# Optimization experiments

Measured on AMD Instinct MI355X. Metric: run time of the kernel, lower is better.

Reference implementation:

```python
import jax, jax.numpy as jnp
import numpy as np

NEG_SLOPE = 0.2


def gat_conv(x, src, dst, n, W, a_src, a_dst, b):
    # x: [N, Din], W: [Din, Dout], a_src/a_dst: [Dout], b: [Dout]
    h = x @ W                                   # [N, Dout]
    alpha_src = h @ a_src                       # [N] score contribution of source nodes
    alpha_dst = h @ a_dst                       # [N]
    e = jax.nn.leaky_relu(alpha_src[src] + alpha_dst[dst], NEG_SLOPE)  # [E]
    # segment softmax over destination nodes (every node has a self-loop -> no empty segs)
    m = jax.ops.segment_max(e, dst, num_segments=n)
    p = jnp.exp(e - m[dst])
    denom = jax.ops.segment_sum(p, dst, num_segments=n)
    coeff = p / denom[dst]                      # [E]
    out = jax.ops.segment_sum(h[src] * coeff[:, None], dst, num_segments=n)
    return out + b


def setup_inputs() -> dict:
    key = jax.random.key(0)
    ks = jax.random.split(key, 16)
    N, E, D_IN, D_H, C = 50000, 800000, 256, 256, 10
    x = jax.random.normal(ks[0], (N, D_IN), dtype=jnp.float32)
    edge_index = jax.random.randint(ks[1], (2, E), 0, N, dtype=jnp.int64)
    s = 0.1
    params = {
        "W1": jax.random.normal(ks[2], (D_IN, D_H), jnp.float32) * s,
        "a_src1": jax.random.normal(ks[3], (D_H,), jnp.float32) * s,
        "a_dst1": jax.random.normal(ks[4], (D_H,), jnp.float32) * s,
        "b1": jnp.zeros((D_H,), jnp.float32),
        "W2": jax.random.normal(ks[5], (D_H, D_H), jnp.float32) * s,
        "a_src2": jax.random.normal(ks[6], (D_H,), jnp.float32) * s,
        "a_dst2": jax.random.normal(ks[7], (D_H,), jnp.float32) * s,
        "b2": jnp.zeros((D_H,), jnp.float32),
        "W3": jax.random.normal(ks[8], (D_H, C), jnp.float32) * s,
        "a_src3": jax.random.normal(ks[9], (C,), jnp.float32) * s,
        "a_dst3": jax.random.normal(ks[10], (C,), jnp.float32) * s,
        "b3": jnp.zeros((C,), jnp.float32),
    }
    return {"x": x, "edge_index": edge_index, **params}


def reference(x, edge_index, W1, a_src1, a_dst1, b1, W2, a_src2, a_dst2, b2,
              W3, a_src3, a_dst3, b3):
    n = x.shape[0]
    # PyG GATConv default add_self_loops=True
    loops = jnp.arange(n, dtype=edge_index.dtype)
    src = jnp.concatenate([edge_index[0], loops])
    dst = jnp.concatenate([edge_index[1], loops])
    h = gat_conv(x, src, dst, n, W1, a_src1, a_dst1, b1)
    h = jax.nn.relu(h)
    h = gat_conv(h, src, dst, n, W2, a_src2, a_dst2, b2)
    h = jax.nn.relu(h)
    out = gat_conv(h, src, dst, n, W3, a_src3, a_dst3, b3)
    return out
```

## Files before the change

kernel.cpp:

```cpp
#include <hip/hip_runtime.h>
#include <math.h>

#define N_NODES 50000
#define N_EDGES 800000
#define EP (N_EDGES + N_NODES)
#define NEG_SLOPE 0.2f
#define SCAN_BLOCKS ((N_NODES + 255) / 256)

typedef short short8 __attribute__((ext_vector_type(8)));
typedef float float4_ __attribute__((ext_vector_type(4)));

__device__ __forceinline__ unsigned short f2bf(float f) {
  unsigned int u = __float_as_uint(f);
  u = (u + 0x7FFFu + ((u >> 16) & 1u)) >> 16;
  return (unsigned short)u;
}
__device__ __forceinline__ float bf2f(unsigned int us) {
  return __uint_as_float(us << 16);
}
__device__ __forceinline__ unsigned int pack2(float lo, float hi) {
  return (unsigned int)f2bf(lo) | ((unsigned int)f2bf(hi) << 16);
}

__device__ __forceinline__ int permc(int p) {
  return ((p & 0xE) << 4) | ((p & 1) << 4) | (p >> 4);
}


template <int PERM>
__global__ void cvt_wf_kernel(const float* __restrict__ W, unsigned short* __restrict__ Wf) {
  int t = blockIdx.x * 256 + threadIdx.x;
  int f = t >> 6, lane = t & 63;
  int nt = f >> 3, k0t = f & 7;
  int lm = lane & 15, kg = lane >> 4;
  int kbase = k0t * 32 + kg * 8;
  int n = nt * 16 + lm;
  short8 v;
#pragma unroll
  for (int j = 0; j < 8; ++j) {
    int k = PERM ? permc(kbase + j) : (kbase + j);
    v[j] = (short)f2bf(W[(size_t)k * 256 + n]);
  }
  ((short8*)Wf)[t] = v;
}

__global__ void cvt_wf3_kernel(const float* __restrict__ W3, unsigned short* __restrict__ Wf3) {
  int t = blockIdx.x * 256 + threadIdx.x;
  int k0t = t >> 6, lane = t & 63;
  int lm = lane & 15, kg = lane >> 4;
  int kbase = k0t * 32 + kg * 8;
  short8 v;
#pragma unroll
  for (int j = 0; j < 8; ++j) {
    int k = permc(kbase + j);
    v[j] = (lm < 10) ? (short)f2bf(W3[(size_t)k * 10 + lm]) : (short)0;
  }
  ((short8*)Wf3)[t] = v;
}

__global__ void permute_bias_kernel(const float* __restrict__ b1, const float* __restrict__ b2,
                                    float* __restrict__ pb1, float* __restrict__ pb2) {
  int p = threadIdx.x;
  int c = permc(p);
  pb1[p] = b1[c];
  pb2[p] = b2[c];
}


__global__ void count_kernel(const int* __restrict__ ei, int* __restrict__ cnt) {
  int e = blockIdx.x * 256 + threadIdx.x;
  if (e >= EP) return;
  int dst = (e < N_EDGES) ? ei[N_EDGES + e] : (e - N_EDGES);
  atomicAdd(&cnt[dst], 1);
}

__global__ void scan1_kernel(const int* __restrict__ cnt, int* __restrict__ off,
                             int* __restrict__ bsum) {
  int i = blockIdx.x * 256 + threadIdx.x;
  int v = (i < N_NODES) ? cnt[i] : 0;
  int lane = threadIdx.x & 63, w = threadIdx.x >> 6;
  int x = v;
  for (int o = 1; o < 64; o <<= 1) { int y = __shfl_up(x, o); if (lane >= o) x += y; }
  __shared__ int wsum[4];
  if (lane == 63) wsum[w] = x;
  __syncthreads();
  int add = 0;
  for (int k = 0; k < w; ++k) add += wsum[k];
  if (i < N_NODES) off[i] = x - v + add;
  if (threadIdx.x == 255) bsum[blockIdx.x] = add + x;
}

__global__ void scan2_kernel(int* __restrict__ bsum, int* __restrict__ bpre,
                             int* __restrict__ off) {
  int t = threadIdx.x;
  int v = (t < SCAN_BLOCKS) ? bsum[t] : 0;
  int lane = t & 63, w = t >> 6;
  int x = v;
  for (int o = 1; o < 64; o <<= 1) { int y = __shfl_up(x, o); if (lane >= o) x += y; }
  __shared__ int wsum[4];
  if (lane == 63) wsum[w] = x;
  __syncthreads();
  int add = 0;
  for (int k = 0; k < w; ++k) add += wsum[k];
  if (t < SCAN_BLOCKS) bpre[t] = x - v + add;
  if (t == 255) off[N_NODES] = add + x;
}

__global__ void scan3_kernel(int* __restrict__ off, const int* __restrict__ bpre) {
  int i = blockIdx.x * 256 + threadIdx.x;
  if (i < N_NODES) off[i] += bpre[blockIdx.x];
}

__global__ void scatter_kernel(const int* __restrict__ ei, const int* __restrict__ off,
                               int* __restrict__ cnt, int* __restrict__ esrc) {
  int e = blockIdx.x * 256 + threadIdx.x;
  if (e >= EP) return;
  int src, dst;
  if (e < N_EDGES) { src = ei[e]; dst = ei[N_EDGES + e]; }
  else { src = dst = e - N_EDGES; }
  int pos = off[dst] + atomicAdd(&cnt[dst], 1);
  esrc[pos] = src;
}


template <int AF32>
__global__ __launch_bounds__(512, 2) void gemm_mfma4(const void* __restrict__ Av,
                                                     const uint4* __restrict__ Wf,
                                                     unsigned short* __restrict__ C,
                                                     const float* __restrict__ asrc,
                                                     const float* __restrict__ adst,
                                                     float* __restrict__ as_,
                                                     float* __restrict__ ad_, int M) {
  __shared__ uint4 Bl[8192];
  int tid = threadIdx.x;
#pragma unroll
  for (int i = 0; i < 16; ++i) Bl[i * 512 + tid] = Wf[i * 512 + tid];
  int wave = tid >> 6, lane = tid & 63;
  int lm = lane & 15, kg = lane >> 4;
  int row0 = blockIdx.x * 256 + wave * 32;
  int ar0 = row0 + lm, ar1 = row0 + 16 + lm;
  if (ar0 >= M) ar0 = M - 1;
  if (ar1 >= M) ar1 = M - 1;
  float4_ acc0[16], acc1[16];
#pragma unroll
  for (int i = 0; i < 16; ++i) { acc0[i] = (float4_){0, 0, 0, 0}; acc1[i] = (float4_){0, 0, 0, 0}; }
  __syncthreads();
  const short8* Bf = (const short8*)Bl;
  for (int k0t = 0; k0t < 8; ++k0t) {
    int k0 = k0t * 32;
    short8 a0, a1;
    if (AF32) {
      const float* A = (const float*)Av;
      const float* p0 = A + (size_t)ar0 * 256 + kg * 8 + k0;
      const float* p1 = A + (size_t)ar1 * 256 + kg * 8 + k0;
      float4 f0 = *(const float4*)p0, f1 = *(const float4*)(p0 + 4);
      float4 g0 = *(const float4*)p1, g1 = *(const float4*)(p1 + 4);
      a0 = (short8){(short)f2bf(f0.x), (short)f2bf(f0.y), (short)f2bf(f0.z), (short)f2bf(f0.w),
                    (short)f2bf(f1.x), (short)f2bf(f1.y), (short)f2bf(f1.z), (short)f2bf(f1.w)};
      a1 = (short8){(short)f2bf(g0.x), (short)f2bf(g0.y), (short)f2bf(g0.z), (short)f2bf(g0.w),
                    (short)f2bf(g1.x), (short)f2bf(g1.y), (short)f2bf(g1.z), (short)f2bf(g1.w)};
    } else {
      const unsigned short* A = (const unsigned short*)Av;
      a0 = *(const short8*)(A + (size_t)ar0 * 256 + kg * 8 + k0);
      a1 = *(const short8*)(A + (size_t)ar1 * 256 + kg * 8 + k0);
    }
#pragma unroll
    for (int nt = 0; nt < 16; ++nt) {
      short8 b = Bf[(nt * 8 + k0t) * 64 + lane];
      acc0[nt] = __builtin_amdgcn_mfma_f32_16x16x32_bf16(a0, b, acc0[nt], 0, 0, 0);
      acc1[nt] = __builtin_amdgcn_mfma_f32_16x16x32_bf16(a1, b, acc1[nt], 0, 0, 0);
    }
  }
  float avs[16], avd[16];
#pragma unroll
  for (int nt = 0; nt < 16; ++nt) { avs[nt] = asrc[nt * 16 + lm]; avd[nt] = adst[nt * 16 + lm]; }
#pragma unroll
  for (int g = 0; g < 2; ++g) {
    int rbase = row0 + g * 16 + kg * 4;
#pragma unroll
    for (int i = 0; i < 4; ++i) {
      int r = rbase + i;
      float s = 0.f, dd = 0.f;
      unsigned int u[8];
#pragma unroll
      for (int j = 0; j < 8; ++j) {
        float vlo = g ? acc1[2 * j][i] : acc0[2 * j][i];
        float vhi = g ? acc1[2 * j + 1][i] : acc0[2 * j + 1][i];
        u[j] = pack2(vlo, vhi);
        s += vlo * avs[2 * j] + vhi * avs[2 * j + 1];
        dd += vlo * avd[2 * j] + vhi * avd[2 * j + 1];
      }
      if (r < M) {
        uint4* cp = (uint4*)(C + (size_t)r * 256 + lm * 16);
        cp[0] = (uint4){u[0], u[1], u[2], u[3]};
        cp[1] = (uint4){u[4], u[5], u[6], u[7]};
      }
#pragma unroll
      for (int o = 1; o < 16; o <<= 1) { s += __shfl_xor(s, o); dd += __shfl_xor(dd, o); }
      if (lm == 0 && r < M) { as_[r] = s; ad_[r] = dd; }
    }
  }
}


__global__ __launch_bounds__(256) void gemm_c3_kernel(const unsigned short* __restrict__ X,
                                                      const unsigned short* __restrict__ Wf3,
                                                      const float* __restrict__ asrc,
                                                      const float* __restrict__ adst,
                                                      float* __restrict__ h3,
                                                      float* __restrict__ as_,
                                                      float* __restrict__ ad_, int M) {
  int tid = threadIdx.x;
  int wave = tid >> 6, lane = tid & 63;
  int lm = lane & 15, kg = lane >> 4;
  int row0 = blockIdx.x * 128 + wave * 32;
  int ar0 = row0 + lm, ar1 = row0 + 16 + lm;
  if (ar0 >= M) ar0 = M - 1;
  if (ar1 >= M) ar1 = M - 1;
  short8 bf[8];
#pragma unroll
  for (int k0t = 0; k0t < 8; ++k0t) bf[k0t] = ((const short8*)Wf3)[k0t * 64 + lane];
  float4_ acc0 = (float4_){0, 0, 0, 0}, acc1 = (float4_){0, 0, 0, 0};
#pragma unroll
  for (int k0t = 0; k0t < 8; ++k0t) {
    int k0 = k0t * 32;
    short8 a0 = *(const short8*)(X + (size_t)ar0 * 256 + kg * 8 + k0);
    short8 a1 = *(const short8*)(X + (size_t)ar1 * 256 + kg * 8 + k0);
    acc0 = __builtin_amdgcn_mfma_f32_16x16x32_bf16(a0, bf[k0t], acc0, 0, 0, 0);
    acc1 = __builtin_amdgcn_mfma_f32_16x16x32_bf16(a1, bf[k0t], acc1, 0, 0, 0);
  }
  float avs = (lm < 10) ? asrc[lm] : 0.f;
  float avd = (lm < 10) ? adst[lm] : 0.f;
#pragma unroll
  for (int g = 0; g < 2; ++g) {
    int rbase = row0 + g * 16 + kg * 4;
#pragma unroll
    for (int i = 0; i < 4; ++i) {
      int r = rbase + i;
      float v = g ? acc1[i] : acc0[i];
      if (r < M && lm < 10) h3[(size_t)r * 10 + lm] = v;
      float s = v * avs, dd = v * avd;
#pragma unroll
      for (int o = 1; o < 16; o <<= 1) { s += __shfl_xor(s, o); dd += __shfl_xor(dd, o); }
      if (lm == 0 && r < M) { as_[r] = s; ad_[r] = dd; }
    }
  }
}


__global__ __launch_bounds__(256) void agg_fused_kernel(const int* __restrict__ off,
                                                        const int* __restrict__ esrc,
                                                        const float* __restrict__ as_,
                                                        const float* __restrict__ ad_,
                                                        const unsigned short* __restrict__ h,
                                                        const float* __restrict__ pbias,
                                                        unsigned short* __restrict__ outg) {
  __shared__ int s_src[4][64];
  __shared__ float s_p[4][64];
  int wave = threadIdx.x >> 6, lane = threadIdx.x & 63;
  int pair = lane >> 5, cl = lane & 31;
  int d = blockIdx.x * 4 + wave;
  int s0 = off[d], s1 = off[d + 1];
  float adv = ad_[d];
  const uint4* hp4 = (const uint4*)h;
  float a0 = 0.f, a1 = 0.f, a2 = 0.f, a3 = 0.f, a4 = 0.f, a5 = 0.f, a6 = 0.f, a7 = 0.f;
  float sum = 0.f;
  for (int base = s0; base < s1; base += 64) {
    int m = s1 - base; if (m > 64) m = 64;
    int sv = 0; float p = 0.f;
    if (lane < m) {
      sv = esrc[base + lane];
      float e = as_[sv] + adv;
      e = e > 0.f ? e : NEG_SLOPE * e;
      p = __expf(e);
    }
    s_src[wave][lane] = sv;
    s_p[wave][lane] = p;
    float ps = p;
    for (int o = 32; o; o >>= 1) ps += __shfl_xor(ps, o);
    sum += ps;
    int nb = (m + 1) >> 1;
    int j = 0;
    for (; j + 4 <= nb; j += 4) {
#pragma unroll
      for (int u = 0; u < 4; ++u) {
        int idx = (j + u) * 2 + pair;
        int src = s_src[wave][idx];
        float w = s_p[wave][idx];
        uint4 pv = hp4[(size_t)src * 32 + cl];
        a0 = fmaf(w, bf2f(pv.x & 0xffffu), a0); a1 = fmaf(w, bf2f(pv.x >> 16), a1);
        a2 = fmaf(w, bf2f(pv.y & 0xffffu), a2); a3 = fmaf(w, bf2f(pv.y >> 16), a3);
        a4 = fmaf(w, bf2f(pv.z & 0xffffu), a4); a5 = fmaf(w, bf2f(pv.z >> 16), a5);
        a6 = fmaf(w, bf2f(pv.w & 0xffffu), a6); a7 = fmaf(w, bf2f(pv.w >> 16), a7);
      }
    }
    for (; j < nb; ++j) {
      int idx = j * 2 + pair;
      int src = s_src[wave][idx];
      float w = s_p[wave][idx];
      uint4 pv = hp4[(size_t)src * 32 + cl];
      a0 = fmaf(w, bf2f(pv.x & 0xffffu), a0); a1 = fmaf(w, bf2f(pv.x >> 16), a1);
      a2 = fmaf(w, bf2f(pv.y & 0xffffu), a2); a3 = fmaf(w, bf2f(pv.y >> 16), a3);
      a4 = fmaf(w, bf2f(pv.z & 0xffffu), a4); a5 = fmaf(w, bf2f(pv.z >> 16), a5);
      a6 = fmaf(w, bf2f(pv.w & 0xffffu), a6); a7 = fmaf(w, bf2f(pv.w >> 16), a7);
    }
  }
  a0 += __shfl_xor(a0, 32); a1 += __shfl_xor(a1, 32);
  a2 += __shfl_xor(a2, 32); a3 += __shfl_xor(a3, 32);
  a4 += __shfl_xor(a4, 32); a5 += __shfl_xor(a5, 32);
  a6 += __shfl_xor(a6, 32); a7 += __shfl_xor(a7, 32);
  if (pair == 0) {
    float inv = 1.0f / sum;
    float4 b0 = ((const float4*)pbias)[2 * cl];
    float4 b1 = ((const float4*)pbias)[2 * cl + 1];
    float o0 = fmaxf(fmaf(a0, inv, b0.x), 0.f);
    float o1 = fmaxf(fmaf(a1, inv, b0.y), 0.f);
    float o2 = fmaxf(fmaf(a2, inv, b0.z), 0.f);
    float o3 = fmaxf(fmaf(a3, inv, b0.w), 0.f);
    float o4 = fmaxf(fmaf(a4, inv, b1.x), 0.f);
    float o5 = fmaxf(fmaf(a5, inv, b1.y), 0.f);
    float o6 = fmaxf(fmaf(a6, inv, b1.z), 0.f);
    float o7 = fmaxf(fmaf(a7, inv, b1.w), 0.f);
    uint4 ov = (uint4){pack2(o0, o1), pack2(o2, o3), pack2(o4, o5), pack2(o6, o7)};
    ((uint4*)outg)[(size_t)d * 32 + cl] = ov;
  }
}


__global__ void agg10_fused_kernel(const int* __restrict__ off, const int* __restrict__ esrc,
                                   const float* __restrict__ as_, const float* __restrict__ ad_,
                                   const float* __restrict__ h, const float* __restrict__ bias,
                                   float* __restrict__ out) {
  int gid = blockIdx.x * 256 + threadIdx.x;
  int wid = gid >> 6, lane = threadIdx.x & 63;
  int g = lane >> 4, c = lane & 15;
  int d = wid * 4 + g;
  if (d >= N_NODES) return;
  int s0 = off[d], s1 = off[d + 1];
  float adv = ad_[d];
  float acc = 0.f, sum = 0.f;
  int s = s0;
  for (; s + 2 <= s1; s += 2) {
    int i0 = esrc[s], i1 = esrc[s + 1];
    float e0 = as_[i0] + adv; e0 = e0 > 0.f ? e0 : NEG_SLOPE * e0;
    float e1 = as_[i1] + adv; e1 = e1 > 0.f ? e1 : NEG_SLOPE * e1;
    float h0 = (c < 10) ? h[(size_t)i0 * 10 + c] : 0.f;
    float h1 = (c < 10) ? h[(size_t)i1 * 10 + c] : 0.f;
    float p0 = __expf(e0), p1 = __expf(e1);
    acc = fmaf(p0, h0, acc);
    acc = fmaf(p1, h1, acc);
    sum += p0 + p1;
  }
  if (s < s1) {
    int i0 = esrc[s];
    float e0 = as_[i0] + adv; e0 = e0 > 0.f ? e0 : NEG_SLOPE * e0;
    float p0 = __expf(e0);
    if (c < 10) acc = fmaf(p0, h[(size_t)i0 * 10 + c], acc);
    sum += p0;
  }
  if (c < 10) out[(size_t)d * 10 + c] = fmaf(acc, 1.0f / sum, bias[c]);
}


extern "C" void kernel_launch(void* const* d_in, const int* in_sizes, int n_in,
                              void* d_out, int out_size, void* d_ws, size_t ws_size,
                              hipStream_t stream) {
  const float* x   = (const float*)d_in[0];
  const int*   ei  = (const int*)d_in[1];
  const float* W1  = (const float*)d_in[2];
  const float* as1 = (const float*)d_in[3];
  const float* ad1 = (const float*)d_in[4];
  const float* b1  = (const float*)d_in[5];
  const float* W2  = (const float*)d_in[6];
  const float* as2 = (const float*)d_in[7];
  const float* ad2 = (const float*)d_in[8];
  const float* b2  = (const float*)d_in[9];
  const float* W3  = (const float*)d_in[10];
  const float* as3 = (const float*)d_in[11];
  const float* ad3 = (const float*)d_in[12];
  const float* b3  = (const float*)d_in[13];
  float* out = (float*)d_out;

  char* ws = (char*)d_ws;
  size_t off_b = 0;
  auto alloc = [&](size_t bytes) -> char* {
    char* p = ws + off_b;
    off_b += (bytes + 255) & ~(size_t)255;
    return p;
  };
  unsigned short* hb   = (unsigned short*)alloc((size_t)N_NODES * 256 * 2);
  unsigned short* gb   = (unsigned short*)alloc((size_t)N_NODES * 256 * 2);
  unsigned short* Wf1  = (unsigned short*)alloc(256 * 256 * 2);
  unsigned short* Wf2  = (unsigned short*)alloc(256 * 256 * 2);
  unsigned short* Wf3  = (unsigned short*)alloc(8 * 64 * 8 * 2);
  float* pb1   = (float*)alloc(256 * 4);
  float* pb2   = (float*)alloc(256 * 4);
  float* h3    = (float*)alloc((size_t)N_NODES * 10 * 4);
  float* as_   = (float*)alloc((size_t)N_NODES * 4);
  float* ad_   = (float*)alloc((size_t)N_NODES * 4);
  int*   roff  = (int*)alloc((size_t)(N_NODES + 1) * 4);
  int*   cnt   = (int*)alloc((size_t)N_NODES * 4);
  int*   bsum  = (int*)alloc((size_t)SCAN_BLOCKS * 4);
  int*   bpre  = (int*)alloc((size_t)SCAN_BLOCKS * 4);
  int*   esrc  = (int*)alloc((size_t)EP * 4);

  cvt_wf_kernel<0><<<32, 256, 0, stream>>>(W1, Wf1);
  cvt_wf_kernel<1><<<32, 256, 0, stream>>>(W2, Wf2);
  cvt_wf3_kernel<<<2, 256, 0, stream>>>(W3, Wf3);
  permute_bias_kernel<<<1, 256, 0, stream>>>(b1, b2, pb1, pb2);

  hipMemsetAsync(cnt, 0, N_NODES * 4, stream);
  int eb = (EP + 255) / 256;
  count_kernel<<<eb, 256, 0, stream>>>(ei, cnt);
  scan1_kernel<<<SCAN_BLOCKS, 256, 0, stream>>>(cnt, roff, bsum);
  scan2_kernel<<<1, 256, 0, stream>>>(bsum, bpre, roff);
  scan3_kernel<<<SCAN_BLOCKS, 256, 0, stream>>>(roff, bpre);
  hipMemsetAsync(cnt, 0, N_NODES * 4, stream);
  scatter_kernel<<<eb, 256, 0, stream>>>(ei, roff, cnt, esrc);

  int g4blocks = (N_NODES + 255) / 256;
  int g3blocks = (N_NODES + 127) / 128;
  int ablocks = (N_NODES + 3) / 4;
  int wgrid4 = (N_NODES * 16 + 255) / 256;

  gemm_mfma4<1><<<g4blocks, 512, 0, stream>>>(x, (const uint4*)Wf1, hb, as1, ad1, as_, ad_, N_NODES);
  agg_fused_kernel<<<ablocks, 256, 0, stream>>>(roff, esrc, as_, ad_, hb, pb1, gb);
  gemm_mfma4<0><<<g4blocks, 512, 0, stream>>>(gb, (const uint4*)Wf2, hb, as2, ad2, as_, ad_, N_NODES);
  agg_fused_kernel<<<ablocks, 256, 0, stream>>>(roff, esrc, as_, ad_, hb, pb2, gb);
  gemm_c3_kernel<<<g3blocks, 256, 0, stream>>>(gb, Wf3, as3, ad3, h3, as_, ad_, N_NODES);
  agg10_fused_kernel<<<wgrid4, 256, 0, stream>>>(roff, esrc, as_, ad_, h3, b3, out);
}
```

Baseline: 379.3 us.

## Prefetch GEMM A tiles, pad layer-3 features, rewrite final aggregation per-wave

The MFMA GEMM now loads the next K-slice of A while the current slice's MFMAs run, hiding global load latency. Layer-3 features are stored padded to 16 floats per row so the final aggregation can fetch them as float4. That aggregation is rewritten to one wave per destination node, with edge weights staged in shared memory, 16 edges processed in parallel and a shuffle reduction. The unroll of the hidden-layer aggregation inner loop also goes from 4 to 8. Costs are more registers in the GEMM and extra memory traffic from the padded layout.

```diff
diff --git a/kernel.cpp b/kernel.cpp
--- a/kernel.cpp
+++ b/kernel.cpp
@@ -141,35 +141,36 @@
   int ar0 = row0 + lm, ar1 = row0 + 16 + lm;
   if (ar0 >= M) ar0 = M - 1;
   if (ar1 >= M) ar1 = M - 1;
+
+  auto loadA = [&](int k0t, int ar) -> short8 {
+    if (AF32) {
+      const float* A = (const float*)Av;
+      const float* p = A + (size_t)ar * 256 + kg * 8 + k0t * 32;
+      float4 f0 = *(const float4*)p, f1 = *(const float4*)(p + 4);
+      return (short8){(short)f2bf(f0.x), (short)f2bf(f0.y), (short)f2bf(f0.z), (short)f2bf(f0.w),
+                      (short)f2bf(f1.x), (short)f2bf(f1.y), (short)f2bf(f1.z), (short)f2bf(f1.w)};
+    } else {
+      const unsigned short* A = (const unsigned short*)Av;
+      return *(const short8*)(A + (size_t)ar * 256 + kg * 8 + k0t * 32);
+    }
+  };
+
   float4_ acc0[16], acc1[16];
 #pragma unroll
   for (int i = 0; i < 16; ++i) { acc0[i] = (float4_){0, 0, 0, 0}; acc1[i] = (float4_){0, 0, 0, 0}; }
+  short8 a0 = loadA(0, ar0), a1 = loadA(0, ar1);
   __syncthreads();
   const short8* Bf = (const short8*)Bl;
   for (int k0t = 0; k0t < 8; ++k0t) {
-    int k0 = k0t * 32;
-    short8 a0, a1;
-    if (AF32) {
-      const float* A = (const float*)Av;
-      const float* p0 = A + (size_t)ar0 * 256 + kg * 8 + k0;
-      const float* p1 = A + (size_t)ar1 * 256 + kg * 8 + k0;
-      float4 f0 = *(const float4*)p0, f1 = *(const float4*)(p0 + 4);
-      float4 g0 = *(const float4*)p1, g1 = *(const float4*)(p1 + 4);
-      a0 = (short8){(short)f2bf(f0.x), (short)f2bf(f0.y), (short)f2bf(f0.z), (short)f2bf(f0.w),
-                    (short)f2bf(f1.x), (short)f2bf(f1.y), (short)f2bf(f1.z), (short)f2bf(f1.w)};
-      a1 = (short8){(short)f2bf(g0.x), (short)f2bf(g0.y), (short)f2bf(g0.z), (short)f2bf(g0.w),
-                    (short)f2bf(g1.x), (short)f2bf(g1.y), (short)f2bf(g1.z), (short)f2bf(g1.w)};
-    } else {
-      const unsigned short* A = (const unsigned short*)Av;
-      a0 = *(const short8*)(A + (size_t)ar0 * 256 + kg * 8 + k0);
-      a1 = *(const short8*)(A + (size_t)ar1 * 256 + kg * 8 + k0);
-    }
+    short8 na0, na1;
+    if (k0t < 7) { na0 = loadA(k0t + 1, ar0); na1 = loadA(k0t + 1, ar1); }
 #pragma unroll
     for (int nt = 0; nt < 16; ++nt) {
       short8 b = Bf[(nt * 8 + k0t) * 64 + lane];
       acc0[nt] = __builtin_amdgcn_mfma_f32_16x16x32_bf16(a0, b, acc0[nt], 0, 0, 0);
       acc1[nt] = __builtin_amdgcn_mfma_f32_16x16x32_bf16(a1, b, acc1[nt], 0, 0, 0);
     }
+    a0 = na0; a1 = na1;
   }
   float avs[16], avd[16];
 #pragma unroll
@@ -207,7 +208,7 @@
                                                       const unsigned short* __restrict__ Wf3,
                                                       const float* __restrict__ asrc,
                                                       const float* __restrict__ adst,
-                                                      float* __restrict__ h3,
+                                                      float* __restrict__ h3p,
                                                       float* __restrict__ as_,
                                                       float* __restrict__ ad_, int M) {
   int tid = threadIdx.x;
@@ -238,7 +239,7 @@
     for (int i = 0; i < 4; ++i) {
       int r = rbase + i;
       float v = g ? acc1[i] : acc0[i];
-      if (r < M && lm < 10) h3[(size_t)r * 10 + lm] = v;
+      if (r < M) h3p[(size_t)r * 16 + lm] = v;
       float s = v * avs, dd = v * avd;
 #pragma unroll
       for (int o = 1; o < 16; o <<= 1) { s += __shfl_xor(s, o); dd += __shfl_xor(dd, o); }
@@ -281,9 +282,9 @@
     sum += ps;
     int nb = (m + 1) >> 1;
     int j = 0;
-    for (; j + 4 <= nb; j += 4) {
-#pragma unroll
-      for (int u = 0; u < 4; ++u) {
+    for (; j + 8 <= nb; j += 8) {
+#pragma unroll
+      for (int u = 0; u < 8; ++u) {
         int idx = (j + u) * 2 + pair;
         int src = s_src[wave][idx];
         float w = s_p[wave][idx];
@@ -327,38 +328,63 @@
 }
 
 
-__global__ void agg10_fused_kernel(const int* __restrict__ off, const int* __restrict__ esrc,
-                                   const float* __restrict__ as_, const float* __restrict__ ad_,
-                                   const float* __restrict__ h, const float* __restrict__ bias,
-                                   float* __restrict__ out) {
-  int gid = blockIdx.x * 256 + threadIdx.x;
-  int wid = gid >> 6, lane = threadIdx.x & 63;
-  int g = lane >> 4, c = lane & 15;
-  int d = wid * 4 + g;
+__global__ __launch_bounds__(256) void agg10_fused_kernel(const int* __restrict__ off,
+                                                          const int* __restrict__ esrc,
+                                                          const float* __restrict__ as_,
+                                                          const float* __restrict__ ad_,
+                                                          const float* __restrict__ h3p,
+                                                          const float* __restrict__ bias,
+                                                          float* __restrict__ out) {
+  __shared__ int s_src[4][64];
+  __shared__ float s_p[4][64];
+  int wave = threadIdx.x >> 6, lane = threadIdx.x & 63;
+  int d = blockIdx.x * 4 + wave;
   if (d >= N_NODES) return;
   int s0 = off[d], s1 = off[d + 1];
   float adv = ad_[d];
-  float acc = 0.f, sum = 0.f;
-  int s = s0;
-  for (; s + 2 <= s1; s += 2) {
-    int i0 = esrc[s], i1 = esrc[s + 1];
-    float e0 = as_[i0] + adv; e0 = e0 > 0.f ? e0 : NEG_SLOPE * e0;
-    float e1 = as_[i1] + adv; e1 = e1 > 0.f ? e1 : NEG_SLOPE * e1;
-    float h0 = (c < 10) ? h[(size_t)i0 * 10 + c] : 0.f;
-    float h1 = (c < 10) ? h[(size_t)i1 * 10 + c] : 0.f;
-    float p0 = __expf(e0), p1 = __expf(e1);
-    acc = fmaf(p0, h0, acc);
-    acc = fmaf(p1, h1, acc);
-    sum += p0 + p1;
-  }
-  if (s < s1) {
-    int i0 = esrc[s];
-    float e0 = as_[i0] + adv; e0 = e0 > 0.f ? e0 : NEG_SLOPE * e0;
-    float p0 = __expf(e0);
-    if (c < 10) acc = fmaf(p0, h[(size_t)i0 * 10 + c], acc);
-    sum += p0;
-  }
-  if (c < 10) out[(size_t)d * 10 + c] = fmaf(acc, 1.0f / sum, bias[c]);
+  int er = lane >> 2;
+  int part = lane & 3;
+  float ax = 0.f, ay = 0.f, az = 0.f, aw = 0.f;
+  float sum = 0.f;
+  const float4* hp = (const float4*)h3p;
+  for (int base = s0; base < s1; base += 64) {
+    int m = s1 - base; if (m > 64) m = 64;
+    int sv = 0; float p = 0.f;
+    if (lane < m) {
+      sv = esrc[base + lane];
+      float e = as_[sv] + adv;
+      e = e > 0.f ? e : NEG_SLOPE * e;
+      p = __expf(e);
+    }
+    s_src[wave][lane] = sv;
+    s_p[wave][lane] = p;
+    float ps = p;
+    for (int o = 32; o; o >>= 1) ps += __shfl_xor(ps, o);
+    sum += ps;
+    int ng = (m + 15) >> 4;
+    for (int g = 0; g < ng; ++g) {
+      int idx = g * 16 + er;
+      int src = s_src[wave][idx];
+      float w = s_p[wave][idx];
+      float4 v = hp[(size_t)src * 4 + part];
+      ax = fmaf(w, v.x, ax); ay = fmaf(w, v.y, ay);
+      az = fmaf(w, v.z, az); aw = fmaf(w, v.w, aw);
+    }
+  }
+  for (int o = 4; o < 64; o <<= 1) {
+    ax += __shfl_xor(ax, o); ay += __shfl_xor(ay, o);
+    az += __shfl_xor(az, o); aw += __shfl_xor(aw, o);
+  }
+  if (lane < 3) {
+    float inv = 1.0f / sum;
+    float* op = out + (size_t)d * 10 + 4 * lane;
+    float2 lo = {fmaf(ax, inv, bias[4 * lane]), fmaf(ay, inv, bias[4 * lane + 1])};
+    *(float2*)op = lo;
+    if (lane < 2) {
+      float2 hi = {fmaf(az, inv, bias[4 * lane + 2]), fmaf(aw, inv, bias[4 * lane + 3])};
+      *(float2*)(op + 2) = hi;
+    }
+  }
 }
 
 
@@ -395,7 +421,7 @@
   unsigned short* Wf3  = (unsigned short*)alloc(8 * 64 * 8 * 2);
   float* pb1   = (float*)alloc(256 * 4);
   float* pb2   = (float*)alloc(256 * 4);
-  float* h3    = (float*)alloc((size_t)N_NODES * 10 * 4);
+  float* h3p   = (float*)alloc((size_t)N_NODES * 16 * 4);
   float* as_   = (float*)alloc((size_t)N_NODES * 4);
   float* ad_   = (float*)alloc((size_t)N_NODES * 4);
   int*   roff  = (int*)alloc((size_t)(N_NODES + 1) * 4);
@@ -421,12 +447,11 @@
   int g4blocks = (N_NODES + 255) / 256;
   int g3blocks = (N_NODES + 127) / 128;
   int ablocks = (N_NODES + 3) / 4;
-  int wgrid4 = (N_NODES * 16 + 255) / 256;
 
   gemm_mfma4<1><<<g4blocks, 512, 0, stream>>>(x, (const uint4*)Wf1, hb, as1, ad1, as_, ad_, N_NODES);
   agg_fused_kernel<<<ablocks, 256, 0, stream>>>(roff, esrc, as_, ad_, hb, pb1, gb);
   gemm_mfma4<0><<<g4blocks, 512, 0, stream>>>(gb, (const uint4*)Wf2, hb, as2, ad2, as_, ad_, N_NODES);
   agg_fused_kernel<<<ablocks, 256, 0, stream>>>(roff, esrc, as_, ad_, hb, pb2, gb);
-  gemm_c3_kernel<<<g3blocks, 256, 0, stream>>>(gb, Wf3, as3, ad3, h3, as_, ad_, N_NODES);
-  agg10_fused_kernel<<<wgrid4, 256, 0, stream>>>(roff, esrc, as_, ad_, h3, b3, out);
-}
+  gemm_c3_kernel<<<g3blocks, 256, 0, stream>>>(gb, Wf3, as3, ad3, h3p, as_, ad_, N_NODES);
+  agg10_fused_kernel<<<ablocks, 256, 0, stream>>>(roff, esrc, as_, ad_, h3p, b3, out);
+}
```

New measurement: 411.5 us. +8.5%, slower.
